# Kernel optimization log

Measured on AMD Instinct MI355X. Metric: run time of the kernel, lower is better.

Reference implementation:

```python
import jax, jax.numpy as jnp
import numpy as np

NEAR_THRESHOLD = 0.25
N = 1536          # entities (== max_entities)
D = 768           # d_model
H = 64            # classifier hidden width
NTYPES = 4        # relation types: 0=NEAR, 1=APPROACHING, 2=FLEEING, 3=ABOVE
SPATIAL = 8       # geometric feature dim


def setup_inputs() -> dict:
    key = jax.random.key(0)
    ks = jax.random.split(key, 6)
    entity_embeddings = jax.random.normal(ks[0], (N, D), dtype=jnp.float32)
    positions = jax.random.uniform(ks[1], (N, 3), dtype=jnp.float32)
    prev_positions = jax.random.uniform(ks[2], (N, 3), dtype=jnp.float32)
    in_dim = 2 * D + SPATIAL
    W1 = jax.random.normal(ks[3], (in_dim, H), dtype=jnp.float32) * (1.0 / np.sqrt(in_dim))
    b1 = jnp.zeros((H,), dtype=jnp.float32)
    W2 = jax.random.normal(ks[4], (H, NTYPES), dtype=jnp.float32) * (1.0 / np.sqrt(H))
    b2 = jnp.zeros((NTYPES,), dtype=jnp.float32)
    return {"entity_embeddings": entity_embeddings, "positions": positions,
            "prev_positions": prev_positions, "W1": W1, "b1": b1, "W2": W2, "b2": b2}


def reference(entity_embeddings, positions, prev_positions, W1, b1, W2, b2):
    n, d = entity_embeddings.shape
    velocities = positions - prev_positions
    # pairwise geometry: entry [i, j] corresponds to pair (a=i, b=j)
    rel_pos = positions[None, :, :] - positions[:, None, :]      # (N, N, 3) = pos_b - pos_a
    rel_vel = velocities[None, :, :] - velocities[:, None, :]    # (N, N, 3)
    distance = jnp.linalg.norm(rel_pos, axis=-1)                 # (N, N)
    closing = -(rel_pos * rel_vel).sum(-1) / jnp.maximum(distance, 1e-6)
    vdiff = rel_pos[..., 1]
    # spatial feats = [dx, dy, dz, dist, dvx, dvy, dvz, vertical_diff]
    sp = jnp.concatenate([rel_pos, distance[..., None], rel_vel, vdiff[..., None]], axis=-1)  # (N, N, 8)

    # first Linear on concat([emb_a, emb_b, sp]) decomposed into three projections
    W1a, W1b, W1s = W1[:d], W1[d:2 * d], W1[2 * d:]
    ha = entity_embeddings @ W1a                                  # (N, H)
    hb = entity_embeddings @ W1b                                  # (N, H)
    hidden = jax.nn.relu(ha[:, None, :] + hb[None, :, :]
                         + jnp.einsum('ijs,sh->ijh', sp, W1s) + b1)  # (N, N, H)
    logits = hidden @ W2 + b2                                     # (N, N, 4)
    probs = jax.nn.softmax(logits, axis=-1)
    best_idx = jnp.argmax(probs, axis=-1)
    conf = jnp.max(probs, axis=-1)

    # conditional overrides (same priority order as _classify_pair)
    near = distance < NEAR_THRESHOLD
    appr = ~near & (closing > 0.05)
    flee = ~near & ~appr & (closing < -0.05)
    above = ~near & ~appr & ~flee & (jnp.abs(vdiff) > 0.3) & (distance < 0.5)
    rel_type = jnp.where(near, 0,
               jnp.where(appr, 1,
               jnp.where(flee, 2,
               jnp.where(above, 3, best_idx)))).astype(jnp.int32)
    conf_out = jnp.where(near, jnp.maximum(conf, 0.8),
               jnp.where(appr, jnp.maximum(conf, 0.6),
               jnp.where(flee, jnp.maximum(conf, 0.6),
               jnp.where(above, jnp.maximum(conf, 0.5), conf))))

    upper = jnp.triu(jnp.ones((n, n), dtype=bool), k=1)           # i < j pairs only
    valid = upper & (conf_out > 0.3)
    return rel_type, conf_out, valid
```

## Files before the change

kernel.cpp:

```cpp
#include <hip/hip_runtime.h>

typedef float f4 __attribute__((ext_vector_type(4)));

#define N 1536
#define D 768
#define H 64
#define NN (N * N)

__global__ __launch_bounds__(256) void k1_gemm(
    const float* __restrict__ E, const float* __restrict__ pos,
    const float* __restrict__ ppos, const float* __restrict__ W1,
    const float* __restrict__ b1, float* __restrict__ P, int KC)
{
    __shared__ f4 Es[16][192];

    const int tid = threadIdx.x;
    const int i0  = blockIdx.x * 16;
    const int kcc = blockIdx.y;
    const int k0  = kcc * KC;
    const int kd4 = KC >> 2;

    for (int f = tid; f < 16 * kd4; f += 256) {
        int row = f / kd4;
        int c   = f - row * kd4;
        Es[row][c] = *(const f4*)&E[(size_t)(i0 + row) * D + k0 + c * 4];
    }
    __syncthreads();

    const int h2  = tid & 127;
    const int ig  = tid >> 7;
    const int mat = h2 >> 6;
    const int h   = h2 & 63;
    const float* Wcol = W1 + (size_t)(mat * D + k0) * H + h;

    float acc[8] = {0.f, 0.f, 0.f, 0.f, 0.f, 0.f, 0.f, 0.f};

    for (int kk = 0; kk < KC; kk += 4) {
        float w0 = Wcol[(size_t)(kk + 0) * H];
        float w1 = Wcol[(size_t)(kk + 1) * H];
        float w2 = Wcol[(size_t)(kk + 2) * H];
        float w3 = Wcol[(size_t)(kk + 3) * H];
#pragma unroll
        for (int r = 0; r < 8; ++r) {
            f4 e = Es[ig * 8 + r][kk >> 2];
            acc[r] = fmaf(e.x, w0, acc[r]);
            acc[r] = fmaf(e.y, w1, acc[r]);
            acc[r] = fmaf(e.z, w2, acc[r]);
            acc[r] = fmaf(e.w, w3, acc[r]);
        }
    }

    if (kcc == 0) {
        float wp0 = W1[(size_t)(2 * D + 0) * H + h];
        float wp1 = W1[(size_t)(2 * D + 1) * H + h] + W1[(size_t)(2 * D + 7) * H + h];
        float wp2 = W1[(size_t)(2 * D + 2) * H + h];
        float wv0 = W1[(size_t)(2 * D + 4) * H + h];
        float wv1 = W1[(size_t)(2 * D + 5) * H + h];
        float wv2 = W1[(size_t)(2 * D + 6) * H + h];
        float bb  = b1[h];
#pragma unroll
        for (int r = 0; r < 8; ++r) {
            int i = i0 + ig * 8 + r;
            float px = pos[3 * i], py = pos[3 * i + 1], pz = pos[3 * i + 2];
            float vx = px - ppos[3 * i];
            float vy = py - ppos[3 * i + 1];
            float vz = pz - ppos[3 * i + 2];
            float g = px * wp0 + py * wp1 + pz * wp2 + vx * wv0 + vy * wv1 + vz * wv2;
            acc[r] += (mat == 0) ? (bb - g) : g;
        }
    }

#pragma unroll
    for (int r = 0; r < 8; ++r) {
        int i = i0 + ig * 8 + r;
        P[(size_t)(kcc * 128 + h2) * N + i] = acc[r];
    }
}

__global__ __launch_bounds__(256) void k2_main(
    const float* __restrict__ P, int nkc,
    const float* __restrict__ W1, const float* __restrict__ W2,
    const float* __restrict__ b2, const float* __restrict__ pos,
    const float* __restrict__ ppos, float* __restrict__ out)
{
    __shared__ f4 As[64][16];
    __shared__ f4 Bs[64][16];
    __shared__ float w3s[64];
    __shared__ f4 W2s[64];
    __shared__ float pis[64][3], vis[64][3], pjs[64][3], vjs[64][3];

    const int tid = threadIdx.x;
    const int i0 = blockIdx.y * 64;
    const int j0 = blockIdx.x * 64;

    for (int g = 0; g < 4; ++g) {
        int f = g * 256 + tid;
        int h = f >> 4;
        int c = f & 15;
        f4 sa = {0.f, 0.f, 0.f, 0.f};
        f4 sb = {0.f, 0.f, 0.f, 0.f};
        for (int kc = 0; kc < nkc; ++kc) {
            sa += *(const f4*)&P[(size_t)(kc * 128 + h) * N + i0 + c * 4];
            sb += *(const f4*)&P[(size_t)(kc * 128 + 64 + h) * N + j0 + c * 4];
        }
        As[h][c] = sa;
        Bs[h][c] = sb;
    }
    if (tid < 64) {
        w3s[tid] = W1[(size_t)(2 * D + 3) * H + tid];
        W2s[tid] = *(const f4*)&W2[tid * 4];
        int i = i0 + tid;
        float px = pos[3 * i], py = pos[3 * i + 1], pz = pos[3 * i + 2];
        pis[tid][0] = px; pis[tid][1] = py; pis[tid][2] = pz;
        vis[tid][0] = px - ppos[3 * i];
        vis[tid][1] = py - ppos[3 * i + 1];
        vis[tid][2] = pz - ppos[3 * i + 2];
    } else if (tid < 128) {
        int t = tid - 64;
        int j = j0 + t;
        float px = pos[3 * j], py = pos[3 * j + 1], pz = pos[3 * j + 2];
        pjs[t][0] = px; pjs[t][1] = py; pjs[t][2] = pz;
        vjs[t][0] = px - ppos[3 * j];
        vjs[t][1] = py - ppos[3 * j + 1];
        vjs[t][2] = pz - ppos[3 * j + 2];
    }
    __syncthreads();

    const int tx = tid & 15;
    const int ty = tid >> 4;

    float dist[16];
    {
#pragma clang fp contract(off)
#pragma unroll
        for (int a = 0; a < 4; ++a) {
#pragma unroll
            for (int b = 0; b < 4; ++b) {
                int il = ty * 4 + a, jl = tx * 4 + b;
                float dx = pjs[jl][0] - pis[il][0];
                float dy = pjs[jl][1] - pis[il][1];
                float dz = pjs[jl][2] - pis[il][2];
                float s = dx * dx;
                s = s + dy * dy;
                s = s + dz * dz;
                dist[a * 4 + b] = sqrtf(s);
            }
        }
    }

    f4 acc[16];
#pragma unroll
    for (int q = 0; q < 16; ++q) acc[q] = (f4){0.f, 0.f, 0.f, 0.f};

#pragma unroll 8
    for (int h = 0; h < 64; ++h) {
        f4 A4 = As[h][ty];
        f4 B4 = Bs[h][tx];
        float w3h = w3s[h];
        f4 w2r = W2s[h];
#pragma unroll
        for (int a = 0; a < 4; ++a) {
#pragma unroll
            for (int b = 0; b < 4; ++b) {
                float hid = fmaf(dist[a * 4 + b], w3h, A4[a] + B4[b]);
                hid = fmaxf(hid, 0.f);
                acc[a * 4 + b] += hid * w2r;
            }
        }
    }

    const f4 b2v = *(const f4*)b2;

#pragma unroll
    for (int a = 0; a < 4; ++a) {
        int i = i0 + ty * 4 + a;
        f4 rt4, cf4, vl4;
#pragma unroll
        for (int b = 0; b < 4; ++b) {
            int j = j0 + tx * 4 + b;
            int il = ty * 4 + a, jl = tx * 4 + b;
            float dd = dist[a * 4 + b];
            float dy, closing;
            {
#pragma clang fp contract(off)
                float dx = pjs[jl][0] - pis[il][0];
                dy       = pjs[jl][1] - pis[il][1];
                float dz = pjs[jl][2] - pis[il][2];
                float rvx = vjs[jl][0] - vis[il][0];
                float rvy = vjs[jl][1] - vis[il][1];
                float rvz = vjs[jl][2] - vis[il][2];
                float dot = dx * rvx;
                dot = dot + dy * rvy;
                dot = dot + dz * rvz;
                closing = -dot / fmaxf(dd, 1e-6f);
            }
            f4 l = acc[a * 4 + b] + b2v;
            float mx = l.x; int bidx = 0;
            if (l.y > mx) { mx = l.y; bidx = 1; }
            if (l.z > mx) { mx = l.z; bidx = 2; }
            if (l.w > mx) { mx = l.w; bidx = 3; }
            float s = expf(l.x - mx);
            s += expf(l.y - mx);
            s += expf(l.z - mx);
            s += expf(l.w - mx);
            float conf = 1.0f / s;

            bool near = dd < 0.25f;
            bool appr = !near && (closing > 0.05f);
            bool flee = !near && !appr && (closing < -0.05f);
            bool above = !near && !appr && !flee && (fabsf(dy) > 0.3f) && (dd < 0.5f);
            int rt = near ? 0 : appr ? 1 : flee ? 2 : above ? 3 : bidx;
            float co = near  ? fmaxf(conf, 0.8f)
                     : appr  ? fmaxf(conf, 0.6f)
                     : flee  ? fmaxf(conf, 0.6f)
                     : above ? fmaxf(conf, 0.5f)
                             : conf;
            float vd = ((j > i) && (co > 0.3f)) ? 1.0f : 0.0f;
            rt4[b] = (float)rt;
            cf4[b] = co;
            vl4[b] = vd;
        }
        int col = j0 + tx * 4;
        *(f4*)&out[(size_t)i * N + col]            = rt4;
        *(f4*)&out[(size_t)NN + (size_t)i * N + col]  = cf4;
        *(f4*)&out[(size_t)2 * NN + (size_t)i * N + col] = vl4;
    }
}

extern "C" void kernel_launch(void* const* d_in, const int* in_sizes, int n_in,
                              void* d_out, int out_size, void* d_ws, size_t ws_size,
                              hipStream_t stream)
{
    const float* E    = (const float*)d_in[0];
    const float* pos  = (const float*)d_in[1];
    const float* ppos = (const float*)d_in[2];
    const float* W1   = (const float*)d_in[3];
    const float* b1   = (const float*)d_in[4];
    const float* W2   = (const float*)d_in[5];
    const float* b2   = (const float*)d_in[6];
    float* out = (float*)d_out;
    float* P   = (float*)d_ws;

    int nkc = (ws_size >= (size_t)4 * 128 * N * 4) ? 4 : 1;
    int KC  = D / nkc;

    dim3 g1(N / 16, nkc);
    k1_gemm<<<g1, 256, 0, stream>>>(E, pos, ppos, W1, b1, P, KC);

    dim3 g2(N / 64, N / 64);
    k2_main<<<g2, 256, 0, stream>>>(P, nkc, W1, W2, b2, pos, ppos, out);
}
```

Measured before the change: 138.2 us.

## Halve pair-kernel tile to 32x64 with packed f2 FMA and vectorize projection GEMM

```diff
diff --git a/kernel.cpp b/kernel.cpp
--- a/kernel.cpp
+++ b/kernel.cpp
@@ -1,6 +1,7 @@
 #include <hip/hip_runtime.h>
 
 typedef float f4 __attribute__((ext_vector_type(4)));
+typedef float f2 __attribute__((ext_vector_type(2)));
 
 #define N 1536
 #define D 768
@@ -12,68 +13,75 @@
     const float* __restrict__ ppos, const float* __restrict__ W1,
     const float* __restrict__ b1, float* __restrict__ P, int KC)
 {
-    __shared__ f4 Es[16][192];
+    __shared__ float Es[16][192];
 
     const int tid = threadIdx.x;
     const int i0  = blockIdx.x * 16;
     const int kcc = blockIdx.y;
     const int k0  = kcc * KC;
-    const int kd4 = KC >> 2;
-
-    for (int f = tid; f < 16 * kd4; f += 256) {
-        int row = f / kd4;
-        int c   = f - row * kd4;
-        Es[row][c] = *(const f4*)&E[(size_t)(i0 + row) * D + k0 + c * 4];
-    }
-    __syncthreads();
-
-    const int h2  = tid & 127;
-    const int ig  = tid >> 7;
-    const int mat = h2 >> 6;
-    const int h   = h2 & 63;
-    const float* Wcol = W1 + (size_t)(mat * D + k0) * H + h;
-
-    float acc[8] = {0.f, 0.f, 0.f, 0.f, 0.f, 0.f, 0.f, 0.f};
-
-    for (int kk = 0; kk < KC; kk += 4) {
-        float w0 = Wcol[(size_t)(kk + 0) * H];
-        float w1 = Wcol[(size_t)(kk + 1) * H];
-        float w2 = Wcol[(size_t)(kk + 2) * H];
-        float w3 = Wcol[(size_t)(kk + 3) * H];
-#pragma unroll
-        for (int r = 0; r < 8; ++r) {
-            f4 e = Es[ig * 8 + r][kk >> 2];
-            acc[r] = fmaf(e.x, w0, acc[r]);
-            acc[r] = fmaf(e.y, w1, acc[r]);
-            acc[r] = fmaf(e.z, w2, acc[r]);
-            acc[r] = fmaf(e.w, w3, acc[r]);
+
+    const int hg  = tid & 31;
+    const int h0  = hg * 4;
+    const int mat = h0 >> 6;
+    const int hc  = h0 & 63;
+    const int rp  = tid >> 5;
+    const float* Wbase = W1 + (size_t)(mat * D + k0) * H + hc;
+
+    f4 acc0 = {0.f, 0.f, 0.f, 0.f};
+    f4 acc1 = {0.f, 0.f, 0.f, 0.f};
+
+    for (int ks = 0; ks < KC; ks += 192) {
+        if (ks) __syncthreads();
+        for (int f = tid; f < 16 * 48; f += 256) {
+            int row = f / 48, c = f - row * 48;
+            *(f4*)&Es[row][c * 4] =
+                *(const f4*)&E[(size_t)(i0 + row) * D + k0 + ks + c * 4];
+        }
+        __syncthreads();
+
+        const float* Wc  = Wbase + (size_t)ks * H;
+        const float* e0p = Es[2 * rp];
+        const float* e1p = Es[2 * rp + 1];
+        for (int kk = 0; kk < 192; kk += 8) {
+#pragma unroll
+            for (int u = 0; u < 8; ++u) {
+                f4 w = *(const f4*)&Wc[(size_t)(kk + u) * H];
+                float e0 = e0p[kk + u], e1 = e1p[kk + u];
+                acc0 = __builtin_elementwise_fma((f4){e0, e0, e0, e0}, w, acc0);
+                acc1 = __builtin_elementwise_fma((f4){e1, e1, e1, e1}, w, acc1);
+            }
         }
     }
 
     if (kcc == 0) {
-        float wp0 = W1[(size_t)(2 * D + 0) * H + h];
-        float wp1 = W1[(size_t)(2 * D + 1) * H + h] + W1[(size_t)(2 * D + 7) * H + h];
-        float wp2 = W1[(size_t)(2 * D + 2) * H + h];
-        float wv0 = W1[(size_t)(2 * D + 4) * H + h];
-        float wv1 = W1[(size_t)(2 * D + 5) * H + h];
-        float wv2 = W1[(size_t)(2 * D + 6) * H + h];
-        float bb  = b1[h];
-#pragma unroll
-        for (int r = 0; r < 8; ++r) {
-            int i = i0 + ig * 8 + r;
+        const float* Ws = W1 + (size_t)2 * D * H + hc;
+        f4 wp0 = *(const f4*)&Ws[0 * H];
+        f4 wp1 = *(const f4*)&Ws[1 * H] + *(const f4*)&Ws[7 * H];
+        f4 wp2 = *(const f4*)&Ws[2 * H];
+        f4 wv0 = *(const f4*)&Ws[4 * H];
+        f4 wv1 = *(const f4*)&Ws[5 * H];
+        f4 wv2 = *(const f4*)&Ws[6 * H];
+        f4 bb  = *(const f4*)&b1[hc];
+#pragma unroll
+        for (int r = 0; r < 2; ++r) {
+            int i = i0 + 2 * rp + r;
             float px = pos[3 * i], py = pos[3 * i + 1], pz = pos[3 * i + 2];
             float vx = px - ppos[3 * i];
             float vy = py - ppos[3 * i + 1];
             float vz = pz - ppos[3 * i + 2];
-            float g = px * wp0 + py * wp1 + pz * wp2 + vx * wv0 + vy * wv1 + vz * wv2;
-            acc[r] += (mat == 0) ? (bb - g) : g;
-        }
-    }
-
-#pragma unroll
-    for (int r = 0; r < 8; ++r) {
-        int i = i0 + ig * 8 + r;
-        P[(size_t)(kcc * 128 + h2) * N + i] = acc[r];
+            f4 g = px * wp0 + py * wp1 + pz * wp2 + vx * wv0 + vy * wv1 + vz * wv2;
+            f4 add = (mat == 0) ? (bb - g) : g;
+            if (r == 0) acc0 += add; else acc1 += add;
+        }
+    }
+
+#pragma unroll
+    for (int r = 0; r < 2; ++r) {
+        int i = i0 + 2 * rp + r;
+        f4 a = r ? acc1 : acc0;
+#pragma unroll
+        for (int c = 0; c < 4; ++c)
+            P[(size_t)(kcc * 128 + h0 + c) * N + i] = a[c];
     }
 }
 
@@ -83,103 +91,133 @@
     const float* __restrict__ b2, const float* __restrict__ pos,
     const float* __restrict__ ppos, float* __restrict__ out)
 {
-    __shared__ f4 As[64][16];
+    __shared__ float As[64][32];
     __shared__ f4 Bs[64][16];
     __shared__ float w3s[64];
     __shared__ f4 W2s[64];
-    __shared__ float pis[64][3], vis[64][3], pjs[64][3], vjs[64][3];
+    __shared__ float pis[32][3], vis[32][3], pjs[64][3], vjs[64][3];
 
     const int tid = threadIdx.x;
-    const int i0 = blockIdx.y * 64;
+    const int i0 = blockIdx.y * 32;
     const int j0 = blockIdx.x * 64;
 
+#pragma unroll
+    for (int g = 0; g < 2; ++g) {
+        int f = g * 256 + tid;
+        int h = f >> 3, c = f & 7;
+        f4 s = {0.f, 0.f, 0.f, 0.f};
+        for (int kc = 0; kc < nkc; ++kc)
+            s += *(const f4*)&P[(size_t)(kc * 128 + h) * N + i0 + c * 4];
+        *(f4*)&As[h][c * 4] = s;
+    }
+#pragma unroll
     for (int g = 0; g < 4; ++g) {
         int f = g * 256 + tid;
-        int h = f >> 4;
-        int c = f & 15;
-        f4 sa = {0.f, 0.f, 0.f, 0.f};
-        f4 sb = {0.f, 0.f, 0.f, 0.f};
-        for (int kc = 0; kc < nkc; ++kc) {
-            sa += *(const f4*)&P[(size_t)(kc * 128 + h) * N + i0 + c * 4];
-            sb += *(const f4*)&P[(size_t)(kc * 128 + 64 + h) * N + j0 + c * 4];
-        }
-        As[h][c] = sa;
-        Bs[h][c] = sb;
+        int h = f >> 4, c = f & 15;
+        f4 s = {0.f, 0.f, 0.f, 0.f};
+        for (int kc = 0; kc < nkc; ++kc)
+            s += *(const f4*)&P[(size_t)(kc * 128 + 64 + h) * N + j0 + c * 4];
+        Bs[h][c] = s;
     }
     if (tid < 64) {
         w3s[tid] = W1[(size_t)(2 * D + 3) * H + tid];
         W2s[tid] = *(const f4*)&W2[tid * 4];
-        int i = i0 + tid;
+        int j = j0 + tid;
+        float px = pos[3 * j], py = pos[3 * j + 1], pz = pos[3 * j + 2];
+        pjs[tid][0] = px; pjs[tid][1] = py; pjs[tid][2] = pz;
+        vjs[tid][0] = px - ppos[3 * j];
+        vjs[tid][1] = py - ppos[3 * j + 1];
+        vjs[tid][2] = pz - ppos[3 * j + 2];
+    } else if (tid < 96) {
+        int t = tid - 64;
+        int i = i0 + t;
         float px = pos[3 * i], py = pos[3 * i + 1], pz = pos[3 * i + 2];
-        pis[tid][0] = px; pis[tid][1] = py; pis[tid][2] = pz;
-        vis[tid][0] = px - ppos[3 * i];
-        vis[tid][1] = py - ppos[3 * i + 1];
-        vis[tid][2] = pz - ppos[3 * i + 2];
-    } else if (tid < 128) {
-        int t = tid - 64;
-        int j = j0 + t;
-        float px = pos[3 * j], py = pos[3 * j + 1], pz = pos[3 * j + 2];
-        pjs[t][0] = px; pjs[t][1] = py; pjs[t][2] = pz;
-        vjs[t][0] = px - ppos[3 * j];
-        vjs[t][1] = py - ppos[3 * j + 1];
-        vjs[t][2] = pz - ppos[3 * j + 2];
+        pis[t][0] = px; pis[t][1] = py; pis[t][2] = pz;
+        vis[t][0] = px - ppos[3 * i];
+        vis[t][1] = py - ppos[3 * i + 1];
+        vis[t][2] = pz - ppos[3 * i + 2];
     }
     __syncthreads();
 
     const int tx = tid & 15;
     const int ty = tid >> 4;
 
-    float dist[16];
+    float dist[2][4];
     {
 #pragma clang fp contract(off)
 #pragma unroll
-        for (int a = 0; a < 4; ++a) {
+        for (int a = 0; a < 2; ++a) {
 #pragma unroll
             for (int b = 0; b < 4; ++b) {
-                int il = ty * 4 + a, jl = tx * 4 + b;
+                int il = ty * 2 + a, jl = tx * 4 + b;
                 float dx = pjs[jl][0] - pis[il][0];
                 float dy = pjs[jl][1] - pis[il][1];
                 float dz = pjs[jl][2] - pis[il][2];
                 float s = dx * dx;
                 s = s + dy * dy;
                 s = s + dz * dz;
-                dist[a * 4 + b] = sqrtf(s);
-            }
-        }
-    }
-
-    f4 acc[16];
-#pragma unroll
-    for (int q = 0; q < 16; ++q) acc[q] = (f4){0.f, 0.f, 0.f, 0.f};
+                dist[a][b] = sqrtf(s);
+            }
+        }
+    }
+
+    f2 d2[2][2];
+#pragma unroll
+    for (int a = 0; a < 2; ++a)
+#pragma unroll
+        for (int p = 0; p < 2; ++p)
+            d2[a][p] = (f2){dist[a][2 * p], dist[a][2 * p + 1]};
+
+    f2 acc[2][2][4];
+#pragma unroll
+    for (int a = 0; a < 2; ++a)
+#pragma unroll
+        for (int p = 0; p < 2; ++p)
+#pragma unroll
+            for (int l = 0; l < 4; ++l)
+                acc[a][p][l] = (f2){0.f, 0.f};
 
 #pragma unroll 8
     for (int h = 0; h < 64; ++h) {
-        f4 A4 = As[h][ty];
+        f2 Ai = *(const f2*)&As[h][ty * 2];
         f4 B4 = Bs[h][tx];
         float w3h = w3s[h];
         f4 w2r = W2s[h];
-#pragma unroll
-        for (int a = 0; a < 4; ++a) {
-#pragma unroll
-            for (int b = 0; b < 4; ++b) {
-                float hid = fmaf(dist[a * 4 + b], w3h, A4[a] + B4[b]);
-                hid = fmaxf(hid, 0.f);
-                acc[a * 4 + b] += hid * w2r;
-            }
-        }
-    }
-
-    const f4 b2v = *(const f4*)b2;
-
-#pragma unroll
-    for (int a = 0; a < 4; ++a) {
-        int i = i0 + ty * 4 + a;
+        f2 w3v = (f2){w3h, w3h};
+        f2 wl0 = (f2){w2r.x, w2r.x};
+        f2 wl1 = (f2){w2r.y, w2r.y};
+        f2 wl2 = (f2){w2r.z, w2r.z};
+        f2 wl3 = (f2){w2r.w, w2r.w};
+#pragma unroll
+        for (int a = 0; a < 2; ++a) {
+            f2 Aa = (f2){Ai[a], Ai[a]};
+#pragma unroll
+            for (int p = 0; p < 2; ++p) {
+                f2 Bp = (f2){B4[2 * p], B4[2 * p + 1]};
+                f2 pre = Aa + Bp;
+                f2 hid = __builtin_elementwise_fma(d2[a][p], w3v, pre);
+                hid = __builtin_elementwise_max(hid, (f2){0.f, 0.f});
+                acc[a][p][0] = __builtin_elementwise_fma(hid, wl0, acc[a][p][0]);
+                acc[a][p][1] = __builtin_elementwise_fma(hid, wl1, acc[a][p][1]);
+                acc[a][p][2] = __builtin_elementwise_fma(hid, wl2, acc[a][p][2]);
+                acc[a][p][3] = __builtin_elementwise_fma(hid, wl3, acc[a][p][3]);
+            }
+        }
+    }
+
+    const f4 B2v = *(const f4*)b2;
+
+#pragma unroll
+    for (int a = 0; a < 2; ++a) {
+        int il = ty * 2 + a;
+        int i = i0 + il;
         f4 rt4, cf4, vl4;
 #pragma unroll
         for (int b = 0; b < 4; ++b) {
-            int j = j0 + tx * 4 + b;
-            int il = ty * 4 + a, jl = tx * 4 + b;
-            float dd = dist[a * 4 + b];
+            int jl = tx * 4 + b;
+            int j = j0 + jl;
+            int p = b >> 1, ln = b & 1;
+            float dd = dist[a][b];
             float dy, closing;
             {
 #pragma clang fp contract(off)
@@ -194,15 +232,18 @@
                 dot = dot + dz * rvz;
                 closing = -dot / fmaxf(dd, 1e-6f);
             }
-            f4 l = acc[a * 4 + b] + b2v;
-            float mx = l.x; int bidx = 0;
-            if (l.y > mx) { mx = l.y; bidx = 1; }
-            if (l.z > mx) { mx = l.z; bidx = 2; }
-            if (l.w > mx) { mx = l.w; bidx = 3; }
-            float s = expf(l.x - mx);
-            s += expf(l.y - mx);
-            s += expf(l.z - mx);
-            s += expf(l.w - mx);
+            float l0 = acc[a][p][0][ln] + B2v.x;
+            float l1 = acc[a][p][1][ln] + B2v.y;
+            float l2 = acc[a][p][2][ln] + B2v.z;
+            float l3 = acc[a][p][3][ln] + B2v.w;
+            float mx = l0; int bidx = 0;
+            if (l1 > mx) { mx = l1; bidx = 1; }
+            if (l2 > mx) { mx = l2; bidx = 2; }
+            if (l3 > mx) { mx = l3; bidx = 3; }
+            float s = expf(l0 - mx);
+            s += expf(l1 - mx);
+            s += expf(l2 - mx);
+            s += expf(l3 - mx);
             float conf = 1.0f / s;
 
             bool near = dd < 0.25f;
@@ -221,8 +262,8 @@
             vl4[b] = vd;
         }
         int col = j0 + tx * 4;
-        *(f4*)&out[(size_t)i * N + col]            = rt4;
-        *(f4*)&out[(size_t)NN + (size_t)i * N + col]  = cf4;
+        *(f4*)&out[(size_t)i * N + col]                  = rt4;
+        *(f4*)&out[(size_t)NN + (size_t)i * N + col]     = cf4;
         *(f4*)&out[(size_t)2 * NN + (size_t)i * N + col] = vl4;
     }
 }
@@ -247,6 +288,6 @@
     dim3 g1(N / 16, nkc);
     k1_gemm<<<g1, 256, 0, stream>>>(E, pos, ppos, W1, b1, P, KC);
 
-    dim3 g2(N / 64, N / 64);
+    dim3 g2(N / 64, N / 32);
     k2_main<<<g2, 256, 0, stream>>>(P, nkc, W1, W2, b2, pos, ppos, out);
 }
```

Result: faster. 130.2 us (-5.8%).
